# Performance work log

Hardware: AMD Instinct MI355X
Metric: run time of the kernel (lower is better)

## Reference

```python
import jax, jax.numpy as jnp
import numpy as np

B, N, TOKEN_DIM = 8, 1024, 768
H, D = 12, 64  # n_heads, head_dim


def setup_inputs() -> dict:
    key = jax.random.key(0)
    k1, k2, k3, k4 = jax.random.split(key, 4)
    x = jax.random.normal(k1, (B, N, TOKEN_DIM), dtype=jnp.float32)
    # nn.Linear(token_dim, 3*H*D, bias=False); store as (in, out)
    W_qkv = jax.random.normal(k2, (TOKEN_DIM, 3 * H * D), dtype=jnp.float32) * (TOKEN_DIM ** -0.5)
    # nn.Linear(H*D, token_dim) with bias
    W_out = jax.random.normal(k3, (H * D, TOKEN_DIM), dtype=jnp.float32) * ((H * D) ** -0.5)
    b_out = jax.random.normal(k4, (TOKEN_DIM,), dtype=jnp.float32) * 0.01
    return {"x": x, "W_qkv": W_qkv, "W_out": W_out, "b_out": b_out}


def reference(x, W_qkv, W_out, b_out):
    b, n, _ = x.shape
    qkv = x @ W_qkv                              # (B, N, 3*H*D)
    # Faithful to original: reshape directly to (B, 3, H, N, D)
    qkv = qkv.reshape(b, 3, H, n, D)
    q, k, v = qkv[:, 0], qkv[:, 1], qkv[:, 2]    # each (B, H, N, D)
    scale = D ** -0.5
    scores = jnp.einsum('bhnd,bhmd->bhnm', q, k) * scale
    probs = jax.nn.softmax(scores, axis=-1)
    attn = jnp.einsum('bhnm,bhmd->bhnd', probs, v)  # (B, H, N, D)
    attn = attn.transpose(0, 2, 1, 3).reshape(b, n, H * D)
    out = attn @ W_out + b_out                    # dropout p=0.0 is identity
    return out
```

## Files before the change

kernel.cpp:

```cpp
#include <hip/hip_runtime.h>
#include <math.h>

static constexpr int NB   = 8;
static constexpr int SEQ  = 1024;
static constexpr int TD   = 768;
static constexpr int NH   = 12;
static constexpr int HD   = 64;
static constexpr int QKVC = 3 * NH * HD;

static constexpr size_t BATCH_ELEMS = (size_t)SEQ * QKVC;
static constexpr size_t THIRD_ELEMS = (size_t)NH * SEQ * HD;
static constexpr size_t HEAD_ELEMS  = (size_t)SEQ * HD;

typedef __bf16 bf16x8 __attribute__((ext_vector_type(8)));
typedef __bf16 bf16x4 __attribute__((ext_vector_type(4)));
typedef float  f32x4  __attribute__((ext_vector_type(4)));

#define MFMA16(a, b, c) __builtin_amdgcn_mfma_f32_16x16x32_bf16((a), (b), (c), 0, 0, 0)

static constexpr float SCL2E = 0.18033688011112042f;

__global__ __launch_bounds__(256) void cast_f32_bf16(const float* __restrict__ in,
                                                     __bf16* __restrict__ out, int n4) {
  int i = blockIdx.x * 256 + threadIdx.x;
  if (i < n4) {
    float4 v = ((const float4*)in)[i];
    bf16x4 o;
    o[0] = (__bf16)v.x; o[1] = (__bf16)v.y; o[2] = (__bf16)v.z; o[3] = (__bf16)v.w;
    ((bf16x4*)out)[i] = o;
  }
}

__global__ __launch_bounds__(256) void wtrans(const float* __restrict__ W,
                                              __bf16* __restrict__ Wt, int K, int N) {
  __shared__ float T[32 * 33];
  const int tid = threadIdx.x;
  const int k0 = blockIdx.y * 32, n0 = blockIdx.x * 32;
#pragma unroll
  for (int i = 0; i < 4; ++i) {
    int idx = tid + i * 256;
    int kk = idx >> 5, nn = idx & 31;
    T[kk * 33 + nn] = W[(size_t)(k0 + kk) * N + n0 + nn];
  }
  __syncthreads();
#pragma unroll
  for (int i = 0; i < 4; ++i) {
    int idx = tid + i * 256;
    int nn = idx >> 5, kk = idx & 31;
    Wt[(size_t)(n0 + nn) * K + k0 + kk] = (__bf16)T[kk * 33 + nn];
  }
}

__global__ __launch_bounds__(256) void vtrans(const __bf16* __restrict__ qkvb,
                                              __bf16* __restrict__ vtb) {
  const int nt = blockIdx.x;
  const int h = blockIdx.y;
  const int b = blockIdx.z;
  __shared__ __bf16 T[128 * 72];
  const int tid = threadIdx.x;
  const int n0 = nt * 128;
  const __bf16* Vb = qkvb + (size_t)b * BATCH_ELEMS + 2 * THIRD_ELEMS + (size_t)h * HEAD_ELEMS;
#pragma unroll
  for (int i = 0; i < 4; ++i) {
    int ch = tid + i * 256;
    int row = ch >> 3, c8 = ch & 7;
    *(bf16x8*)&T[row * 72 + c8 * 8] = *(const bf16x8*)&Vb[(size_t)(n0 + row) * HD + c8 * 8];
  }
  __syncthreads();
#pragma unroll
  for (int i = 0; i < 4; ++i) {
    int ch = tid + i * 256;
    int d = ch >> 4, n8 = ch & 15;
    bf16x8 v;
#pragma unroll
    for (int j = 0; j < 8; ++j) v[j] = T[(n8 * 8 + j) * 72 + d];
    *(bf16x8*)&vtb[((size_t)((b * NH + h) * HD) + d) * SEQ + n0 + n8 * 8] = v;
  }
}

template <int OUT_BF16>
__global__ __launch_bounds__(256) void gemm_mfma(const __bf16* __restrict__ A,
                                                 const __bf16* __restrict__ Bt,
                                                 const float* __restrict__ bias,
                                                 void* __restrict__ C,
                                                 int M, int N, int K) {
  __shared__ __bf16 As[128 * 40];
  __shared__ __bf16 Bs[128 * 40];
  const int tid = threadIdx.x;
  const int lane = tid & 63;
  const int wid = tid >> 6;
  const int wr = wid >> 1, wc = wid & 1;
  const int r = lane & 15, g = lane >> 4;
  const size_t bm = (size_t)blockIdx.y * 128;
  const size_t bn = (size_t)blockIdx.x * 128;

  f32x4 acc[4][4];
#pragma unroll
  for (int mi = 0; mi < 4; ++mi)
#pragma unroll
    for (int nj = 0; nj < 4; ++nj) acc[mi][nj] = (f32x4){0.f, 0.f, 0.f, 0.f};

  for (int k0 = 0; k0 < K; k0 += 32) {
#pragma unroll
    for (int i = 0; i < 2; ++i) {
      int ch = tid + i * 256;
      int row = ch >> 2, c8 = ch & 3;
      *(bf16x8*)&As[row * 40 + c8 * 8] =
          *(const bf16x8*)&A[(bm + row) * K + k0 + c8 * 8];
      *(bf16x8*)&Bs[row * 40 + c8 * 8] =
          *(const bf16x8*)&Bt[(bn + row) * K + k0 + c8 * 8];
    }
    __syncthreads();
    bf16x8 af[4], bf[4];
#pragma unroll
    for (int mi = 0; mi < 4; ++mi)
      af[mi] = *(const bf16x8*)&As[(wr * 64 + mi * 16 + r) * 40 + g * 8];
#pragma unroll
    for (int nj = 0; nj < 4; ++nj)
      bf[nj] = *(const bf16x8*)&Bs[(wc * 64 + nj * 16 + r) * 40 + g * 8];
#pragma unroll
    for (int mi = 0; mi < 4; ++mi)
#pragma unroll
      for (int nj = 0; nj < 4; ++nj)
        acc[mi][nj] = MFMA16(af[mi], bf[nj], acc[mi][nj]);
    __syncthreads();
  }

  const int orow0 = g * 4;
  const int ocol = r;
#pragma unroll
  for (int mi = 0; mi < 4; ++mi)
#pragma unroll
    for (int nj = 0; nj < 4; ++nj)
#pragma unroll
      for (int reg = 0; reg < 4; ++reg) {
        size_t rrow = bm + wr * 64 + mi * 16 + orow0 + reg;
        size_t ccol = bn + wc * 64 + nj * 16 + ocol;
        float v = acc[mi][nj][reg];
        if (OUT_BF16)
          ((__bf16*)C)[rrow * N + ccol] = (__bf16)v;
        else
          ((float*)C)[rrow * N + ccol] = v + bias[ccol];
      }
}

__global__ __launch_bounds__(256) void attn_mfma(const __bf16* __restrict__ qkvb,
                                                 const __bf16* __restrict__ vtb,
                                                 __bf16* __restrict__ attn2b) {
  const int qt = blockIdx.x;
  const int h = blockIdx.y;
  const int b = blockIdx.z;
  const int tid = threadIdx.x;
  const int lane = tid & 63;
  const int wid = tid >> 6;
  const int c = lane & 15, g = lane >> 4;

  __shared__ __bf16 Ks[64 * 72];
  __shared__ __bf16 Vs[64 * 72];

  const __bf16* Qb = qkvb + (size_t)b * BATCH_ELEMS + (size_t)h * HEAD_ELEMS;
  const __bf16* Kb = Qb + THIRD_ELEMS;
  const __bf16* Vtb = vtb + (size_t)((b * NH + h) * HD) * SEQ;
  const int q0 = qt * 64 + wid * 16;

  bf16x8 qf[2];
#pragma unroll
  for (int f = 0; f < 2; ++f)
    qf[f] = *(const bf16x8*)&Qb[(size_t)(q0 + c) * HD + f * 32 + g * 8];

  f32x4 Oa[4];
#pragma unroll
  for (int db = 0; db < 4; ++db) Oa[db] = (f32x4){0.f, 0.f, 0.f, 0.f};
  float mrow = -3.0e38f, lrow = 0.f;

  const int rbase = ((c >> 2) << 3) | (c & 3);

  for (int kv0 = 0; kv0 < SEQ; kv0 += 64) {
#pragma unroll
    for (int i = 0; i < 2; ++i) {
      int ch = tid + i * 256;
      int row = ch >> 3, c8 = ch & 7;
      *(bf16x8*)&Ks[row * 72 + c8 * 8] =
          *(const bf16x8*)&Kb[(size_t)(kv0 + row) * HD + c8 * 8];
      *(bf16x8*)&Vs[row * 72 + c8 * 8] =
          *(const bf16x8*)&Vtb[(size_t)row * SEQ + kv0 + c8 * 8];
    }
    __syncthreads();

    f32x4 sa[4];
#pragma unroll
    for (int t = 0; t < 4; ++t) sa[t] = (f32x4){0.f, 0.f, 0.f, 0.f};
#pragma unroll
    for (int t = 0; t < 4; ++t) {
      const int krow = rbase + ((t >> 1) << 5) + ((t & 1) << 2);
#pragma unroll
      for (int f = 0; f < 2; ++f) {
        bf16x8 kf = *(const bf16x8*)&Ks[krow * 72 + f * 32 + g * 8];
        sa[t] = MFMA16(kf, qf[f], sa[t]);
      }
    }

    float tm = -3.0e38f;
#pragma unroll
    for (int t = 0; t < 4; ++t)
#pragma unroll
      for (int reg = 0; reg < 4; ++reg) tm = fmaxf(tm, sa[t][reg]);
    tm = fmaxf(tm, __shfl_xor(tm, 16));
    tm = fmaxf(tm, __shfl_xor(tm, 32));
    const float mnew = fmaxf(mrow, tm);
    const float alpha = __builtin_exp2f((mrow - mnew) * SCL2E);
    float rs = 0.f;
    float p[4][4];
#pragma unroll
    for (int t = 0; t < 4; ++t)
#pragma unroll
      for (int reg = 0; reg < 4; ++reg) {
        float pv = __builtin_exp2f((sa[t][reg] - mnew) * SCL2E);
        p[t][reg] = pv;
        rs += pv;
      }
    rs += __shfl_xor(rs, 16);
    rs += __shfl_xor(rs, 32);
    lrow = lrow * alpha + rs;
    mrow = mnew;
#pragma unroll
    for (int db = 0; db < 4; ++db)
#pragma unroll
      for (int reg = 0; reg < 4; ++reg) Oa[db][reg] *= alpha;

    bf16x8 pb[2];
#pragma unroll
    for (int kk = 0; kk < 2; ++kk)
#pragma unroll
      for (int i = 0; i < 4; ++i) {
        pb[kk][i] = (__bf16)p[2 * kk][i];
        pb[kk][4 + i] = (__bf16)p[2 * kk + 1][i];
      }

#pragma unroll
    for (int db = 0; db < 4; ++db)
#pragma unroll
      for (int kk = 0; kk < 2; ++kk) {
        bf16x8 vf = *(const bf16x8*)&Vs[(db * 16 + c) * 72 + kk * 32 + g * 8];
        Oa[db] = MFMA16(vf, pb[kk], Oa[db]);
      }
    __syncthreads();
  }

  const float inv = 1.0f / lrow;
  const size_t rowq = (size_t)(b * SEQ) + q0 + c;
#pragma unroll
  for (int db = 0; db < 4; ++db) {
    bf16x4 o;
#pragma unroll
    for (int reg = 0; reg < 4; ++reg) o[reg] = (__bf16)(Oa[db][reg] * inv);
    *(bf16x4*)&attn2b[rowq * TD + h * HD + db * 16 + g * 4] = o;
  }
}

extern "C" void kernel_launch(void* const* d_in, const int* in_sizes, int n_in,
                              void* d_out, int out_size, void* d_ws,
                              size_t ws_size, hipStream_t stream) {
  const float* x = (const float*)d_in[0];
  const float* W_qkv = (const float*)d_in[1];
  const float* W_out = (const float*)d_in[2];
  const float* b_out = (const float*)d_in[3];
  float* out = (float*)d_out;

  __bf16* xb = (__bf16*)d_ws;
  __bf16* wqkvt = xb + (size_t)NB * SEQ * TD;
  __bf16* woutt = wqkvt + (size_t)QKVC * TD;
  __bf16* qkvb = woutt + (size_t)TD * TD;
  __bf16* vtb = qkvb + (size_t)NB * SEQ * QKVC;
  __bf16* attn2b = vtb + (size_t)NB * NH * HD * SEQ;

  cast_f32_bf16<<<(NB * SEQ * TD / 4 + 255) / 256, 256, 0, stream>>>(x, xb, NB * SEQ * TD / 4);
  wtrans<<<dim3(QKVC / 32, TD / 32), 256, 0, stream>>>(W_qkv, wqkvt, TD, QKVC);
  wtrans<<<dim3(TD / 32, TD / 32), 256, 0, stream>>>(W_out, woutt, TD, TD);

  gemm_mfma<1><<<dim3(QKVC / 128, NB * SEQ / 128), 256, 0, stream>>>(
      xb, wqkvt, nullptr, qkvb, NB * SEQ, QKVC, TD);

  vtrans<<<dim3(SEQ / 128, NH, NB), 256, 0, stream>>>(qkvb, vtb);

  attn_mfma<<<dim3(SEQ / 64, NH, NB), 256, 0, stream>>>(qkvb, vtb, attn2b);

  gemm_mfma<0><<<dim3(TD / 128, NB * SEQ / 128), 256, 0, stream>>>(
      attn2b, woutt, b_out, out, NB * SEQ, TD, TD);
}
```

Baseline: 164.0 us.

## Double-buffer attention K/V tiles in fragment-major LDS and use direct global-to-LDS loads in GEMM

```diff
diff --git a/kernel.cpp b/kernel.cpp
--- a/kernel.cpp
+++ b/kernel.cpp
@@ -19,6 +19,12 @@
 #define MFMA16(a, b, c) __builtin_amdgcn_mfma_f32_16x16x32_bf16((a), (b), (c), 0, 0, 0)
 
 static constexpr float SCL2E = 0.18033688011112042f;
+
+__device__ __forceinline__ void gload_lds16(const void* g, void* l) {
+  __builtin_amdgcn_global_load_lds(
+      (const __attribute__((address_space(1))) unsigned int*)g,
+      (__attribute__((address_space(3))) unsigned int*)l, 16, 0, 0);
+}
 
 __global__ __launch_bounds__(256) void cast_f32_bf16(const float* __restrict__ in,
                                                      __bf16* __restrict__ out, int n4) {
@@ -84,8 +90,8 @@
                                                  const float* __restrict__ bias,
                                                  void* __restrict__ C,
                                                  int M, int N, int K) {
-  __shared__ __bf16 As[128 * 40];
-  __shared__ __bf16 Bs[128 * 40];
+  __shared__ __bf16 As[128 * 32];
+  __shared__ __bf16 Bs[128 * 32];
   const int tid = threadIdx.x;
   const int lane = tid & 63;
   const int wid = tid >> 6;
@@ -94,6 +100,9 @@
   const size_t bm = (size_t)blockIdx.y * 128;
   const size_t bn = (size_t)blockIdx.x * 128;
 
+  const int srow = lane >> 2;
+  const int scol = (lane & 3) * 8;
+
   f32x4 acc[4][4];
 #pragma unroll
   for (int mi = 0; mi < 4; ++mi)
@@ -102,22 +111,19 @@
 
   for (int k0 = 0; k0 < K; k0 += 32) {
 #pragma unroll
-    for (int i = 0; i < 2; ++i) {
-      int ch = tid + i * 256;
-      int row = ch >> 2, c8 = ch & 3;
-      *(bf16x8*)&As[row * 40 + c8 * 8] =
-          *(const bf16x8*)&A[(bm + row) * K + k0 + c8 * 8];
-      *(bf16x8*)&Bs[row * 40 + c8 * 8] =
-          *(const bf16x8*)&Bt[(bn + row) * K + k0 + c8 * 8];
+    for (int j = 0; j < 2; ++j) {
+      const int rowbase = wid * 32 + j * 16;
+      gload_lds16(&A[(bm + rowbase + srow) * K + k0 + scol], &As[rowbase * 32]);
+      gload_lds16(&Bt[(bn + rowbase + srow) * K + k0 + scol], &Bs[rowbase * 32]);
     }
     __syncthreads();
     bf16x8 af[4], bf[4];
 #pragma unroll
     for (int mi = 0; mi < 4; ++mi)
-      af[mi] = *(const bf16x8*)&As[(wr * 64 + mi * 16 + r) * 40 + g * 8];
+      af[mi] = *(const bf16x8*)&As[(wr * 64 + mi * 16 + r) * 32 + g * 8];
 #pragma unroll
     for (int nj = 0; nj < 4; ++nj)
-      bf[nj] = *(const bf16x8*)&Bs[(wc * 64 + nj * 16 + r) * 40 + g * 8];
+      bf[nj] = *(const bf16x8*)&Bs[(wc * 64 + nj * 16 + r) * 32 + g * 8];
 #pragma unroll
     for (int mi = 0; mi < 4; ++mi)
 #pragma unroll
@@ -152,16 +158,28 @@
   const int b = blockIdx.z;
   const int tid = threadIdx.x;
   const int lane = tid & 63;
-  const int wid = tid >> 6;
+  const int w = tid >> 6;
   const int c = lane & 15, g = lane >> 4;
 
-  __shared__ __bf16 Ks[64 * 72];
-  __shared__ __bf16 Vs[64 * 72];
+  __shared__ __bf16 KsF[2][4096];
+  __shared__ __bf16 VsF[2][4096];
 
   const __bf16* Qb = qkvb + (size_t)b * BATCH_ELEMS + (size_t)h * HEAD_ELEMS;
   const __bf16* Kb = Qb + THIRD_ELEMS;
   const __bf16* Vtb = vtb + (size_t)((b * NH + h) * HD) * SEQ;
-  const int q0 = qt * 64 + wid * 16;
+  const int q0 = qt * 64 + w * 16;
+
+  int kOffG[2], vOffG[2], sOffL[2];
+#pragma unroll
+  for (int i = 0; i < 2; ++i) {
+    const int t2f = i * 4 + w;
+    const int t = t2f >> 1, f = t2f & 1;
+    const int krow = ((t >> 1) << 5) | ((c >> 2) << 3) | ((t & 1) << 2) | (c & 3);
+    kOffG[i] = krow * HD + f * 32 + g * 8;
+    const int db = t2f >> 1, kk = t2f & 1;
+    vOffG[i] = (db * 16 + c) * SEQ + kk * 32 + g * 8;
+    sOffL[i] = (t2f * 64 + lane) * 8;
+  }
 
   bf16x8 qf[2];
 #pragma unroll
@@ -171,34 +189,42 @@
   f32x4 Oa[4];
 #pragma unroll
   for (int db = 0; db < 4; ++db) Oa[db] = (f32x4){0.f, 0.f, 0.f, 0.f};
-  float mrow = -3.0e38f, lrow = 0.f;
-
-  const int rbase = ((c >> 2) << 3) | (c & 3);
-
-  for (int kv0 = 0; kv0 < SEQ; kv0 += 64) {
-#pragma unroll
-    for (int i = 0; i < 2; ++i) {
-      int ch = tid + i * 256;
-      int row = ch >> 3, c8 = ch & 7;
-      *(bf16x8*)&Ks[row * 72 + c8 * 8] =
-          *(const bf16x8*)&Kb[(size_t)(kv0 + row) * HD + c8 * 8];
-      *(bf16x8*)&Vs[row * 72 + c8 * 8] =
-          *(const bf16x8*)&Vtb[(size_t)row * SEQ + kv0 + c8 * 8];
+  float mrow = -3.0e38f, mrowS = -3.0e38f * SCL2E, lrow = 0.f;
+
+  bf16x8 kreg[2], vreg[2];
+#pragma unroll
+  for (int i = 0; i < 2; ++i) {
+    kreg[i] = *(const bf16x8*)&Kb[kOffG[i]];
+    vreg[i] = *(const bf16x8*)&Vtb[vOffG[i]];
+  }
+#pragma unroll
+  for (int i = 0; i < 2; ++i) {
+    *(bf16x8*)&KsF[0][sOffL[i]] = kreg[i];
+    *(bf16x8*)&VsF[0][sOffL[i]] = vreg[i];
+  }
+  __syncthreads();
+
+  int cur = 0;
+  for (int it = 0; it < SEQ / 64; ++it) {
+    if (it < SEQ / 64 - 1) {
+      const int kv0 = (it + 1) * 64;
+#pragma unroll
+      for (int i = 0; i < 2; ++i) {
+        kreg[i] = *(const bf16x8*)&Kb[(size_t)kv0 * HD + kOffG[i]];
+        vreg[i] = *(const bf16x8*)&Vtb[kv0 + vOffG[i]];
+      }
     }
-    __syncthreads();
 
     f32x4 sa[4];
 #pragma unroll
     for (int t = 0; t < 4; ++t) sa[t] = (f32x4){0.f, 0.f, 0.f, 0.f};
 #pragma unroll
-    for (int t = 0; t < 4; ++t) {
-      const int krow = rbase + ((t >> 1) << 5) + ((t & 1) << 2);
+    for (int t = 0; t < 4; ++t)
 #pragma unroll
       for (int f = 0; f < 2; ++f) {
-        bf16x8 kf = *(const bf16x8*)&Ks[krow * 72 + f * 32 + g * 8];
+        bf16x8 kf = *(const bf16x8*)&KsF[cur][(t * 2 + f) * 512 + lane * 8];
         sa[t] = MFMA16(kf, qf[f], sa[t]);
       }
-    }
 
     float tm = -3.0e38f;
 #pragma unroll
@@ -207,26 +233,31 @@
       for (int reg = 0; reg < 4; ++reg) tm = fmaxf(tm, sa[t][reg]);
     tm = fmaxf(tm, __shfl_xor(tm, 16));
     tm = fmaxf(tm, __shfl_xor(tm, 32));
-    const float mnew = fmaxf(mrow, tm);
-    const float alpha = __builtin_exp2f((mrow - mnew) * SCL2E);
+    if (!__all(tm <= mrow)) {
+      const float mnew = fmaxf(mrow, tm);
+      const float mnewS = mnew * SCL2E;
+      const float alpha = __builtin_exp2f(mrowS - mnewS);
+      lrow *= alpha;
+#pragma unroll
+      for (int db = 0; db < 4; ++db)
+#pragma unroll
+        for (int reg = 0; reg < 4; ++reg) Oa[db][reg] *= alpha;
+      mrow = mnew;
+      mrowS = mnewS;
+    }
     float rs = 0.f;
     float p[4][4];
 #pragma unroll
     for (int t = 0; t < 4; ++t)
 #pragma unroll
       for (int reg = 0; reg < 4; ++reg) {
-        float pv = __builtin_exp2f((sa[t][reg] - mnew) * SCL2E);
+        float pv = __builtin_exp2f(__builtin_fmaf(sa[t][reg], SCL2E, -mrowS));
         p[t][reg] = pv;
         rs += pv;
       }
     rs += __shfl_xor(rs, 16);
     rs += __shfl_xor(rs, 32);
-    lrow = lrow * alpha + rs;
-    mrow = mnew;
-#pragma unroll
-    for (int db = 0; db < 4; ++db)
-#pragma unroll
-      for (int reg = 0; reg < 4; ++reg) Oa[db][reg] *= alpha;
+    lrow += rs;
 
     bf16x8 pb[2];
 #pragma unroll
@@ -241,10 +272,20 @@
     for (int db = 0; db < 4; ++db)
 #pragma unroll
       for (int kk = 0; kk < 2; ++kk) {
-        bf16x8 vf = *(const bf16x8*)&Vs[(db * 16 + c) * 72 + kk * 32 + g * 8];
+        bf16x8 vf = *(const bf16x8*)&VsF[cur][(db * 2 + kk) * 512 + lane * 8];
         Oa[db] = MFMA16(vf, pb[kk], Oa[db]);
       }
+
+    if (it < SEQ / 64 - 1) {
+      const int nxt = cur ^ 1;
+#pragma unroll
+      for (int i = 0; i < 2; ++i) {
+        *(bf16x8*)&KsF[nxt][sOffL[i]] = kreg[i];
+        *(bf16x8*)&VsF[nxt][sOffL[i]] = vreg[i];
+      }
+    }
     __syncthreads();
+    cur ^= 1;
   }
 
   const float inv = 1.0f / lrow;
```

Measured after the change: 158.0 us. -3.6%, faster.
